# Optimization experiments

Measured on AMD Instinct MI355X. Metric: run time of the kernel, lower is better.

The kernel has to match this reference:

```python
import jax, jax.numpy as jnp
import numpy as np
import math

HEAD_DEPTH = 16
CLIP = 10.0
NEG_INF = 1.0e10
# combined scale: (1/sqrt(head_depth)) * log_50(400)
SCALE = (math.log(400.0) / math.log(50.0)) / math.sqrt(HEAD_DEPTH)


def setup_inputs() -> dict:
    key = jax.random.key(0)
    kq, kk, kv, km = jax.random.split(key, 4)
    B, H, S, D = 4, 8, 2048, HEAD_DEPTH
    Q = jax.random.normal(kq, (B, H, S, D), dtype=jnp.float32)
    K = jax.random.normal(kk, (B, H, S, D), dtype=jnp.float32)
    V = jax.random.normal(kv, (B, H, S, D), dtype=jnp.float32)
    # mask: (B, n_nodes, 1) bool; True -> masked (logit set to -inf)
    mask = jax.random.randint(km, (B, S, 1), 0, 2) == 1
    return {"Q": Q, "K": K, "V": V, "mask": mask}


def reference(Q, K, V, mask):
    # logits: (B, H, q_seq, k_seq)
    logits = jnp.einsum("bhqd,bhkd->bhqk", Q, K) * SCALE
    logits = CLIP * jnp.tanh(logits)  # tanh clip
    # mask[:, None, None, :, 0] -> (B, 1, 1, k_seq), True gets -inf
    m = mask[:, None, None, :, 0]
    logits = jnp.where(m, -NEG_INF, logits)
    probs = jax.nn.softmax(logits, axis=-1)
    return jnp.einsum("bhqk,bhkd->bhqd", probs, V)
```

## Files before the change

kernel.cpp:

```cpp
#include <hip/hip_runtime.h>


typedef __fp16 h2 __attribute__((ext_vector_type(2)));
typedef __fp16 h4 __attribute__((ext_vector_type(4)));
typedef float  f4 __attribute__((ext_vector_type(4)));

#define KROW 20
#define VROW 520

__device__ __forceinline__ float fast_exp2(float x) {
#if __has_builtin(__builtin_amdgcn_exp2f)
    return __builtin_amdgcn_exp2f(x);
#else
    return exp2f(x);
#endif
}

__device__ __forceinline__ float dot2acc(h2 a, float accv) {
#if __has_builtin(__builtin_amdgcn_fdot2)
    const h2 one = {(__fp16)1.0f, (__fp16)1.0f};
    return __builtin_amdgcn_fdot2(a, one, accv, false);
#else
    return accv + (float)a[0] + (float)a[1];
#endif
}

__global__ __launch_bounds__(512, 8) void attn_fwd(
    const float* __restrict__ Qp, const float* __restrict__ Kp,
    const float* __restrict__ Vp, const int* __restrict__ maskp,
    float* __restrict__ out)
{
    __shared__ __align__(16) _Float16 Klds[512 * KROW];
    __shared__ __align__(16) _Float16 Vt[16 * VROW];
    __shared__ __align__(16) float biasf[512];

    const int bid  = blockIdx.x;
    const int bh   = bid >> 5;
    const int qblk = bid & 31;
    const int b    = bh >> 3;
    const int tid  = threadIdx.x;
    const int wave = tid >> 6;
    const int lane = tid & 63;
    const int qt   = wave & 3;
    const int kg   = wave >> 2;
    const int c    = lane & 15;
    const int g    = lane >> 4;

    const size_t base = (size_t)bh * (2048 * 16);
    const int qbase = qblk * 64 + qt * 16;

    const float c1 = 1.1047809f;
    const float c2 = -28.8539008f;

    h4 qfrag;
    {
        f4 qv = *(const f4*)(Qp + base + (size_t)(qbase + c) * 16 + 4 * g);
        h2 lo = __builtin_amdgcn_cvt_pkrtz(c1 * qv[0], c1 * qv[1]);
        h2 hi = __builtin_amdgcn_cvt_pkrtz(c1 * qv[2], c1 * qv[3]);
        qfrag[0] = lo[0]; qfrag[1] = lo[1]; qfrag[2] = hi[0]; qfrag[3] = hi[1];
    }

    f4 acc = {0.f, 0.f, 0.f, 0.f};
    float dsum = 0.f;

    const int kgb = kg * 256;

    for (int round = 0; round < 4; ++round) {
        {
            const float* Kc = Kp + base + (size_t)round * (512 * 16);
            const float* Vc = Vp + base + (size_t)round * (512 * 16);
            #pragma unroll
            for (int j = 0; j < 4; ++j) {
                const int i = j * 512 + tid;
                f4 kv = *(const f4*)(Kc + (size_t)i * 4);
                f4 vv = *(const f4*)(Vc + (size_t)i * 4);
                const int key = i >> 2;
                const int dq  = (i & 3) * 4;
                h2 k0 = __builtin_amdgcn_cvt_pkrtz(kv[0], kv[1]);
                h2 k1 = __builtin_amdgcn_cvt_pkrtz(kv[2], kv[3]);
                h4 kh; kh[0] = k0[0]; kh[1] = k0[1]; kh[2] = k1[0]; kh[3] = k1[1];
                *(h4*)&Klds[key * KROW + dq] = kh;
                #pragma unroll
                for (int e = 0; e < 4; ++e)
                    Vt[(dq + e) * VROW + key] = (_Float16)vv[e];
            }
            biasf[tid] = maskp[(size_t)b * 2048 + round * 512 + tid] ? -60.0f : 0.0f;
        }
        __syncthreads();

        #pragma unroll
        for (int t = 0; t < 16; ++t) {
            const int kb = kgb + t * 16;
            h4 afrag = *(const h4*)&Klds[(kb + c) * KROW + 4 * g];
            f4 s = __builtin_amdgcn_mfma_f32_16x16x16f16(
                afrag, qfrag, (f4){0.f, 0.f, 0.f, 0.f}, 0, 0, 0);

            f4 b4 = *(const f4*)&biasf[kb + 4 * g];
            float p[4];
            #pragma unroll
            for (int r = 0; r < 4; ++r) {
                float tt = fast_exp2(s[r]);
                float w  = __builtin_amdgcn_rcpf(1.0f + tt);
                p[r] = fast_exp2(__builtin_fmaf(c2, w, b4[r]));
            }
            h2 plo = __builtin_amdgcn_cvt_pkrtz(p[0], p[1]);
            h2 phi = __builtin_amdgcn_cvt_pkrtz(p[2], p[3]);
            dsum = dot2acc(plo, dsum);
            dsum = dot2acc(phi, dsum);
            h4 pf; pf[0] = plo[0]; pf[1] = plo[1]; pf[2] = phi[0]; pf[3] = phi[1];

            h4 vfrag = *(const h4*)&Vt[c * VROW + kb + 4 * g];
            acc = __builtin_amdgcn_mfma_f32_16x16x16f16(pf, vfrag, acc, 0, 0, 0);
        }
        __syncthreads();
    }

    dsum += __shfl_xor(dsum, 16);
    dsum += __shfl_xor(dsum, 32);

    float* ex = (float*)Klds;
    const int slot = (qt * 64 + lane) * 5;
    if (kg == 1) {
        ex[slot + 0] = acc[0]; ex[slot + 1] = acc[1];
        ex[slot + 2] = acc[2]; ex[slot + 3] = acc[3];
        ex[slot + 4] = dsum;
    }
    __syncthreads();
    if (kg == 0) {
        const float dT = dsum + ex[slot + 4];
        #pragma unroll
        for (int r = 0; r < 4; ++r) {
            const float denom = __shfl(dT, 4 * g + r);
            out[base + (size_t)(qbase + 4 * g + r) * 16 + c] =
                (acc[r] + ex[slot + r]) / denom;
        }
    }
}

extern "C" void kernel_launch(void* const* d_in, const int* in_sizes, int n_in,
                              void* d_out, int out_size, void* d_ws, size_t ws_size,
                              hipStream_t stream) {
    const float* Q    = (const float*)d_in[0];
    const float* K    = (const float*)d_in[1];
    const float* V    = (const float*)d_in[2];
    const int*   mask = (const int*)d_in[3];
    float* out = (float*)d_out;
    attn_fwd<<<dim3(1024), dim3(512), 0, stream>>>(Q, K, V, mask, out);
}
```

Measured before the change: 110.7 us.

## Pre-convert K/V to fp16 MFMA-fragment layout in workspace, double-buffer LDS

Adds a prep kernel that converts K, V and the mask into fp16 fragments laid out in MFMA order in the workspace, plus a float bias array. Previously each of the 32 query blocks per head redid this conversion. The main kernel then loads contiguous fragments into double-buffered LDS with register prefetch, so global loads overlap compute and the padded, transposed LDS stores go away. The cost is a second launch and a workspace round trip, and the old kernel is kept as a fallback when the workspace is too small.

```diff
diff --git a/kernel.cpp b/kernel.cpp
--- a/kernel.cpp
+++ b/kernel.cpp
@@ -5,8 +5,13 @@
 typedef __fp16 h4 __attribute__((ext_vector_type(4)));
 typedef float  f4 __attribute__((ext_vector_type(4)));
 
-#define KROW 20
-#define VROW 520
+#define SEQ 2048
+#define NBH 32
+#define TPB 128
+#define KWS_BYTES ((size_t)NBH * TPB * 64 * 8)
+#define VWS_BYTES KWS_BYTES
+#define BIAS_BYTES ((size_t)4 * SEQ * 4)
+#define WS_NEEDED (KWS_BYTES + VWS_BYTES + BIAS_BYTES)
 
 __device__ __forceinline__ float fast_exp2(float x) {
 #if __has_builtin(__builtin_amdgcn_exp2f)
@@ -25,14 +30,48 @@
 #endif
 }
 
-__global__ __launch_bounds__(512, 8) void attn_fwd(
-    const float* __restrict__ Qp, const float* __restrict__ Kp,
-    const float* __restrict__ Vp, const int* __restrict__ maskp,
+__global__ __launch_bounds__(256) void attn_prep(
+    const float* __restrict__ Kp, const float* __restrict__ Vp,
+    const int* __restrict__ maskp,
+    __fp16* __restrict__ Kws, __fp16* __restrict__ Vws, float* __restrict__ biasws)
+{
+    const int tid = threadIdx.x;
+    const int T   = blockIdx.x * 4 + (tid >> 6);
+    const int l   = tid & 63;
+    const int bh  = T >> 7;
+    const int t   = T & (TPB - 1);
+    const int c   = l & 15;
+    const int g   = l >> 4;
+    const size_t base = (size_t)bh * (SEQ * 16);
+
+    {
+        f4 kv = *(const f4*)(Kp + base + (size_t)(t * 16 + c) * 16 + 4 * g);
+        h2 k0 = __builtin_amdgcn_cvt_pkrtz(kv[0], kv[1]);
+        h2 k1 = __builtin_amdgcn_cvt_pkrtz(kv[2], kv[3]);
+        h4 kh; kh[0] = k0[0]; kh[1] = k0[1]; kh[2] = k1[0]; kh[3] = k1[1];
+        *(h4*)(Kws + ((size_t)T * 64 + l) * 4) = kh;
+    }
+    {
+        const float* vrow = Vp + base + (size_t)(t * 16 + 4 * g) * 16 + c;
+        h2 p0 = __builtin_amdgcn_cvt_pkrtz(vrow[0],  vrow[16]);
+        h2 p1 = __builtin_amdgcn_cvt_pkrtz(vrow[32], vrow[48]);
+        h4 vh; vh[0] = p0[0]; vh[1] = p0[1]; vh[2] = p1[0]; vh[3] = p1[1];
+        *(h4*)(Vws + ((size_t)T * 64 + l) * 4) = vh;
+    }
+    if (blockIdx.x < 32) {
+        const int idx = blockIdx.x * 256 + tid;
+        biasws[idx] = maskp[idx] ? -60.0f : 0.0f;
+    }
+}
+
+__global__ __launch_bounds__(512, 8) void attn_v4(
+    const float* __restrict__ Qp, const __fp16* __restrict__ Kws,
+    const __fp16* __restrict__ Vws, const float* __restrict__ biasws,
     float* __restrict__ out)
 {
-    __shared__ __align__(16) _Float16 Klds[512 * KROW];
-    __shared__ __align__(16) _Float16 Vt[16 * VROW];
-    __shared__ __align__(16) float biasf[512];
+    __shared__ __align__(16) _Float16 Kbuf[2][4096];
+    __shared__ __align__(16) _Float16 Vbuf[2][4096];
+    __shared__ __align__(16) float    Bbuf[2][256];
 
     const int bid  = blockIdx.x;
     const int bh   = bid >> 5;
@@ -46,11 +85,10 @@
     const int c    = lane & 15;
     const int g    = lane >> 4;
 
-    const size_t base = (size_t)bh * (2048 * 16);
-    const int qbase = qblk * 64 + qt * 16;
-
-    const float c1 = 1.1047809f;
-    const float c2 = -28.8539008f;
+    const size_t base  = (size_t)bh * (SEQ * 16);
+    const int    qbase = qblk * 64 + qt * 16;
+    const float  c1 = 1.1047809f;
+    const float  c2 = -28.8539008f;
 
     h4 qfrag;
     {
@@ -60,9 +98,128 @@
         qfrag[0] = lo[0]; qfrag[1] = lo[1]; qfrag[2] = hi[0]; qfrag[3] = hi[1];
     }
 
+    const f4* ksrc = (const f4*)(Kws + (size_t)bh * TPB * 256);
+    const f4* vsrc = (const f4*)(Vws + (size_t)bh * TPB * 256);
+    const float* bsrc = biasws + (size_t)b * SEQ;
+
+    f4 kpre = ksrc[tid];
+    f4 vpre = vsrc[tid];
+    float bpre = (tid < 256) ? bsrc[tid] : 0.0f;
+    *(f4*)&Kbuf[0][tid * 8] = kpre;
+    *(f4*)&Vbuf[0][tid * 8] = vpre;
+    if (tid < 256) Bbuf[0][tid] = bpre;
+    kpre = ksrc[512 + tid];
+    vpre = vsrc[512 + tid];
+    if (tid < 256) bpre = bsrc[256 + tid];
+    __syncthreads();
+
     f4 acc = {0.f, 0.f, 0.f, 0.f};
     float dsum = 0.f;
 
+    for (int r = 0; r < 8; ++r) {
+        const int cb = r & 1, nb = (r + 1) & 1;
+        if (r < 7) {
+            *(f4*)&Kbuf[nb][tid * 8] = kpre;
+            *(f4*)&Vbuf[nb][tid * 8] = vpre;
+            if (tid < 256) Bbuf[nb][tid] = bpre;
+        }
+        if (r < 6) {
+            kpre = ksrc[(r + 2) * 512 + tid];
+            vpre = vsrc[(r + 2) * 512 + tid];
+            if (tid < 256) bpre = bsrc[(r + 2) * 256 + tid];
+        }
+
+        const _Float16* Kc = &Kbuf[cb][kg * 2048];
+        const _Float16* Vc = &Vbuf[cb][kg * 2048];
+        const float*    Bc = &Bbuf[cb][kg * 128];
+
+        #pragma unroll
+        for (int t = 0; t < 8; ++t) {
+            h4 afrag = *(const h4*)(Kc + t * 256 + lane * 4);
+            f4 s = __builtin_amdgcn_mfma_f32_16x16x16f16(
+                afrag, qfrag, (f4){0.f, 0.f, 0.f, 0.f}, 0, 0, 0);
+
+            f4 b4 = *(const f4*)(Bc + t * 16 + 4 * g);
+            float p[4];
+            #pragma unroll
+            for (int i = 0; i < 4; ++i) {
+                float tt = fast_exp2(s[i]);
+                float w  = __builtin_amdgcn_rcpf(1.0f + tt);
+                p[i] = fast_exp2(__builtin_fmaf(c2, w, b4[i]));
+            }
+            h2 plo = __builtin_amdgcn_cvt_pkrtz(p[0], p[1]);
+            h2 phi = __builtin_amdgcn_cvt_pkrtz(p[2], p[3]);
+            dsum = dot2acc(plo, dsum);
+            dsum = dot2acc(phi, dsum);
+            h4 pf; pf[0] = plo[0]; pf[1] = plo[1]; pf[2] = phi[0]; pf[3] = phi[1];
+
+            h4 vfrag = *(const h4*)(Vc + t * 256 + lane * 4);
+            acc = __builtin_amdgcn_mfma_f32_16x16x16f16(pf, vfrag, acc, 0, 0, 0);
+        }
+        __syncthreads();
+    }
+
+    dsum += __shfl_xor(dsum, 16);
+    dsum += __shfl_xor(dsum, 32);
+
+    float* ex = (float*)&Kbuf[0][0];
+    const int slot = (qt * 64 + lane) * 5;
+    if (kg == 1) {
+        ex[slot + 0] = acc[0]; ex[slot + 1] = acc[1];
+        ex[slot + 2] = acc[2]; ex[slot + 3] = acc[3];
+        ex[slot + 4] = dsum;
+    }
+    __syncthreads();
+    if (kg == 0) {
+        const float dT = dsum + ex[slot + 4];
+        #pragma unroll
+        for (int i = 0; i < 4; ++i) {
+            const float denom = __shfl(dT, 4 * g + i);
+            out[base + (size_t)(qbase + 4 * g + i) * 16 + c] =
+                (acc[i] + ex[slot + i]) / denom;
+        }
+    }
+}
+
+#define KROW 20
+#define VROW 520
+
+__global__ __launch_bounds__(512, 8) void attn_fwd_v3(
+    const float* __restrict__ Qp, const float* __restrict__ Kp,
+    const float* __restrict__ Vp, const int* __restrict__ maskp,
+    float* __restrict__ out)
+{
+    __shared__ __align__(16) _Float16 Klds[512 * KROW];
+    __shared__ __align__(16) _Float16 Vt[16 * VROW];
+    __shared__ __align__(16) float biasf[512];
+
+    const int bid  = blockIdx.x;
+    const int bh   = bid >> 5;
+    const int qblk = bid & 31;
+    const int b    = bh >> 3;
+    const int tid  = threadIdx.x;
+    const int wave = tid >> 6;
+    const int lane = tid & 63;
+    const int qt   = wave & 3;
+    const int kg   = wave >> 2;
+    const int c    = lane & 15;
+    const int g    = lane >> 4;
+
+    const size_t base = (size_t)bh * (SEQ * 16);
+    const int qbase = qblk * 64 + qt * 16;
+    const float c1 = 1.1047809f;
+    const float c2 = -28.8539008f;
+
+    h4 qfrag;
+    {
+        f4 qv = *(const f4*)(Qp + base + (size_t)(qbase + c) * 16 + 4 * g);
+        h2 lo = __builtin_amdgcn_cvt_pkrtz(c1 * qv[0], c1 * qv[1]);
+        h2 hi = __builtin_amdgcn_cvt_pkrtz(c1 * qv[2], c1 * qv[3]);
+        qfrag[0] = lo[0]; qfrag[1] = lo[1]; qfrag[2] = hi[0]; qfrag[3] = hi[1];
+    }
+
+    f4 acc = {0.f, 0.f, 0.f, 0.f};
+    float dsum = 0.f;
     const int kgb = kg * 256;
 
     for (int round = 0; round < 4; ++round) {
@@ -84,7 +241,7 @@
                 for (int e = 0; e < 4; ++e)
                     Vt[(dq + e) * VROW + key] = (_Float16)vv[e];
             }
-            biasf[tid] = maskp[(size_t)b * 2048 + round * 512 + tid] ? -60.0f : 0.0f;
+            biasf[tid] = maskp[(size_t)b * SEQ + round * 512 + tid] ? -60.0f : 0.0f;
         }
         __syncthreads();
 
@@ -94,21 +251,19 @@
             h4 afrag = *(const h4*)&Klds[(kb + c) * KROW + 4 * g];
             f4 s = __builtin_amdgcn_mfma_f32_16x16x16f16(
                 afrag, qfrag, (f4){0.f, 0.f, 0.f, 0.f}, 0, 0, 0);
-
             f4 b4 = *(const f4*)&biasf[kb + 4 * g];
             float p[4];
             #pragma unroll
-            for (int r = 0; r < 4; ++r) {
-                float tt = fast_exp2(s[r]);
+            for (int i = 0; i < 4; ++i) {
+                float tt = fast_exp2(s[i]);
                 float w  = __builtin_amdgcn_rcpf(1.0f + tt);
-                p[r] = fast_exp2(__builtin_fmaf(c2, w, b4[r]));
+                p[i] = fast_exp2(__builtin_fmaf(c2, w, b4[i]));
             }
             h2 plo = __builtin_amdgcn_cvt_pkrtz(p[0], p[1]);
             h2 phi = __builtin_amdgcn_cvt_pkrtz(p[2], p[3]);
             dsum = dot2acc(plo, dsum);
             dsum = dot2acc(phi, dsum);
             h4 pf; pf[0] = plo[0]; pf[1] = plo[1]; pf[2] = phi[0]; pf[3] = phi[1];
-
             h4 vfrag = *(const h4*)&Vt[c * VROW + kb + 4 * g];
             acc = __builtin_amdgcn_mfma_f32_16x16x16f16(pf, vfrag, acc, 0, 0, 0);
         }
@@ -129,10 +284,10 @@
     if (kg == 0) {
         const float dT = dsum + ex[slot + 4];
         #pragma unroll
-        for (int r = 0; r < 4; ++r) {
-            const float denom = __shfl(dT, 4 * g + r);
-            out[base + (size_t)(qbase + 4 * g + r) * 16 + c] =
-                (acc[r] + ex[slot + r]) / denom;
+        for (int i = 0; i < 4; ++i) {
+            const float denom = __shfl(dT, 4 * g + i);
+            out[base + (size_t)(qbase + 4 * g + i) * 16 + c] =
+                (acc[i] + ex[slot + i]) / denom;
         }
     }
 }
@@ -145,5 +300,14 @@
     const float* V    = (const float*)d_in[2];
     const int*   mask = (const int*)d_in[3];
     float* out = (float*)d_out;
-    attn_fwd<<<dim3(1024), dim3(512), 0, stream>>>(Q, K, V, mask, out);
-}
+
+    if (ws_size >= WS_NEEDED) {
+        __fp16* Kws = (__fp16*)d_ws;
+        __fp16* Vws = (__fp16*)((char*)d_ws + KWS_BYTES);
+        float*  Bws = (float*)((char*)d_ws + KWS_BYTES + VWS_BYTES);
+        attn_prep<<<dim3(1024), dim3(256), 0, stream>>>(K, V, mask, Kws, Vws, Bws);
+        attn_v4<<<dim3(1024), dim3(512), 0, stream>>>(Q, Kws, Vws, Bws, out);
+    } else {
+        attn_fwd_v3<<<dim3(1024), dim3(512), 0, stream>>>(Q, K, V, mask, out);
+    }
+}
```

New measurement: 106.6 us. 3.7% less time.
